# Performance work log

Hardware: AMD Instinct MI355X
Metric: run time of the kernel (lower is better)

Reference implementation:

```python
import jax, jax.numpy as jnp
import numpy as np

B, N, D_IN, D_ATTN, D_OUT = 8, 2048, 2048, 64, 2048

def setup_inputs() -> dict:
    key = jax.random.key(0)
    ks = jax.random.split(key, 5)
    x = jax.random.normal(ks[0], (B, N, D_IN), dtype=jnp.float32)
    s_qkv = 1.0 / np.sqrt(D_IN)   # torch nn.Linear default init bound
    W_qkv = jax.random.uniform(ks[1], (D_IN, 3 * D_ATTN), jnp.float32, -s_qkv, s_qkv)
    b_qkv = jax.random.uniform(ks[2], (3 * D_ATTN,), jnp.float32, -s_qkv, s_qkv)
    s_p = 1.0 / np.sqrt(D_ATTN)
    W_proj = jax.random.uniform(ks[3], (D_ATTN, D_OUT), jnp.float32, -s_p, s_p)
    b_proj = jax.random.uniform(ks[4], (D_OUT,), jnp.float32, -s_p, s_p)
    return {"x": x, "W_qkv": W_qkv, "b_qkv": b_qkv, "W_proj": W_proj, "b_proj": b_proj}

def reference(x, W_qkv, b_qkv, W_proj, b_proj):
    # qkv projection: [B,N,3*D_ATTN]
    qkv = x @ W_qkv + b_qkv
    q, k, v = jnp.split(qkv, 3, axis=-1)  # each [B,N,D_ATTN]
    scale = jax.lax.rsqrt(jnp.float32(D_ATTN))
    w = jnp.einsum('bnd,bmd->bnm', q, k) * scale  # [B,N,N]
    a = jax.nn.softmax(w, axis=-1)
    ctx = jnp.einsum('bnm,bmd->bnd', a, v)        # [B,N,D_ATTN]
    return ctx @ W_proj + b_proj                   # [B,N,D_OUT]
```

## Files before the change

### kernel.cpp

```cpp
#include <hip/hip_runtime.h>

typedef __bf16 bf16x8 __attribute__((ext_vector_type(8)));
typedef unsigned short u16x8 __attribute__((ext_vector_type(8)));
typedef unsigned short u16x4 __attribute__((ext_vector_type(4)));
typedef float  f32x4  __attribute__((ext_vector_type(4)));

#define QSCALE 0.1803368801111204f

__device__ __forceinline__ unsigned short f2bf(float f) {
  unsigned int u = __float_as_uint(f);
  u = u + 0x7fffu + ((u >> 16) & 1u);
  return (unsigned short)(u >> 16);
}

#define GLD16(src, dst)                                                        \
  __builtin_amdgcn_global_load_lds(                                            \
      (const __attribute__((address_space(1))) void*)(src),                    \
      (__attribute__((address_space(3))) void*)(dst), 16, 0, 0)


__global__ __launch_bounds__(256) void k_tr_wq(const float* __restrict__ W,
                                               unsigned short* __restrict__ WT) {
  __shared__ float tile[64][193];
  const int t = threadIdx.x;
  const int k0 = blockIdx.x * 64;
#pragma unroll
  for (int i = 0; i < 12; ++i) {
    int u = i * 256 + t;
    int row = u / 48, c4 = u % 48;
    float4 v = *(const float4*)(W + (size_t)(k0 + row) * 192 + c4 * 4);
    tile[row][c4 * 4 + 0] = v.x; tile[row][c4 * 4 + 1] = v.y;
    tile[row][c4 * 4 + 2] = v.z; tile[row][c4 * 4 + 3] = v.w;
  }
  __syncthreads();
#pragma unroll
  for (int i = 0; i < 6; ++i) {
    int u = i * 256 + t;
    int c = u >> 3, k8 = (u & 7) * 8;
    u16x8 h;
#pragma unroll
    for (int j = 0; j < 8; ++j) h[j] = f2bf(tile[k8 + j][c]);
    *(u16x8*)(WT + (size_t)c * 2048 + k0 + k8) = h;
  }
}

__global__ __launch_bounds__(256) void k_tr_wp(const float* __restrict__ W,
                                               unsigned short* __restrict__ WT) {
  __shared__ float tile[64][65];
  const int t = threadIdx.x;
  const int n0 = blockIdx.x * 64;
#pragma unroll
  for (int i = 0; i < 4; ++i) {
    int u = i * 256 + t;
    int d = u >> 4, c4 = u & 15;
    float4 v = *(const float4*)(W + (size_t)d * 2048 + n0 + c4 * 4);
    tile[d][c4 * 4 + 0] = v.x; tile[d][c4 * 4 + 1] = v.y;
    tile[d][c4 * 4 + 2] = v.z; tile[d][c4 * 4 + 3] = v.w;
  }
  __syncthreads();
#pragma unroll
  for (int i = 0; i < 2; ++i) {
    int u = i * 256 + t;
    int n = u >> 3, d8 = (u & 7) * 8;
    u16x8 h;
#pragma unroll
    for (int j = 0; j < 8; ++j) h[j] = f2bf(tile[d8 + j][n0 ? n : n]);
    h[0] = f2bf(tile[d8 + 0][n]); h[1] = f2bf(tile[d8 + 1][n]);
    h[2] = f2bf(tile[d8 + 2][n]); h[3] = f2bf(tile[d8 + 3][n]);
    h[4] = f2bf(tile[d8 + 4][n]); h[5] = f2bf(tile[d8 + 5][n]);
    h[6] = f2bf(tile[d8 + 6][n]); h[7] = f2bf(tile[d8 + 7][n]);
    *(u16x8*)(WT + (size_t)(n0 + n) * 64 + d8) = h;
  }
}

__global__ __launch_bounds__(512) void k_qkv(const float* __restrict__ x,
                                             const unsigned short* __restrict__ wqT,
                                             const float* __restrict__ b_qkv,
                                             unsigned short* __restrict__ qb,
                                             unsigned short* __restrict__ kb,
                                             unsigned short* __restrict__ vt) {
  __shared__ __align__(16) char lds[65536];
  const int t = threadIdx.x;
  const int lane = t & 63, w = t >> 6;
  const int l15 = lane & 15, l4 = lane >> 4;
  const int wm = w >> 2, wn = w & 3;
  const int m0 = blockIdx.x * 64;

  const int arow = t >> 3;
  const int akc  = (t & 7) * 8;
  const float* xrow = x + (size_t)(m0 + arow) * 2048 + akc;
  const int aoff = arow * 128 + ((akc * 2) ^ ((arow & 7) << 4));

  f32x4 acc[2][3] = {};
  float4 a0, a1;

  auto issueA = [&](int kt) {
    a0 = *(const float4*)(xrow + kt * 64);
    a1 = *(const float4*)(xrow + kt * 64 + 4);
  };
  auto writeA = [&](int d) {
    u16x8 h;
    h[0] = f2bf(a0.x); h[1] = f2bf(a0.y); h[2] = f2bf(a0.z); h[3] = f2bf(a0.w);
    h[4] = f2bf(a1.x); h[5] = f2bf(a1.y); h[6] = f2bf(a1.z); h[7] = f2bf(a1.w);
    *(u16x8*)(lds + d * 8192 + aoff) = h;
  };
  auto stageB = [&](int kt, int d) {
    char* bbase = lds + 16384 + d * 24576;
#pragma unroll
    for (int p = 0; p < 3; ++p) {
      int L = p * 8192 + (w << 10) + (lane << 4);
      int row = L >> 7;
      int cb = (L & 127) ^ ((row & 7) << 4);
      GLD16((const char*)wqT + (size_t)row * 4096 + kt * 128 + cb,
            bbase + p * 8192 + (w << 10));
    }
  };
  auto compute = [&](int d) {
    const char* aB = lds + d * 8192;
    const char* bB = lds + 16384 + d * 24576;
#pragma unroll
    for (int kk = 0; kk < 2; ++kk) {
      int cb = kk * 64 + l4 * 16;
      bf16x8 af[2], bfr[3];
#pragma unroll
      for (int m = 0; m < 2; ++m) {
        int r = wm * 32 + m * 16 + l15;
        af[m] = *(const bf16x8*)(aB + r * 128 + (cb ^ ((r & 7) << 4)));
      }
#pragma unroll
      for (int n = 0; n < 3; ++n) {
        int r = wn * 48 + n * 16 + l15;
        bfr[n] = *(const bf16x8*)(bB + r * 128 + (cb ^ ((r & 7) << 4)));
      }
#pragma unroll
      for (int m = 0; m < 2; ++m)
#pragma unroll
        for (int n = 0; n < 3; ++n)
          acc[m][n] = __builtin_amdgcn_mfma_f32_16x16x32_bf16(af[m], bfr[n], acc[m][n], 0, 0, 0);
    }
  };

  issueA(0); stageB(0, 0); writeA(0);
  __syncthreads();
  int d = 0;
  for (int kt = 0; kt < 32; ++kt) {
    if (kt < 31) { issueA(kt + 1); stageB(kt + 1, d ^ 1); }
    compute(d);
    if (kt < 31) writeA(d ^ 1);
    __syncthreads();
    d ^= 1;
  }

#pragma unroll
  for (int m = 0; m < 2; ++m)
#pragma unroll
    for (int n = 0; n < 3; ++n) {
      int c = wn * 48 + n * 16 + l15;
      int j = c >> 6, cc = c & 63;
      float bias = b_qkv[c];
      int grow0 = m0 + wm * 32 + m * 16 + l4 * 4;
      if (j == 0) {
#pragma unroll
        for (int r = 0; r < 4; ++r)
          qb[(size_t)(grow0 + r) * 64 + cc] = f2bf((acc[m][n][r] + bias) * QSCALE);
      } else if (j == 1) {
#pragma unroll
        for (int r = 0; r < 4; ++r)
          kb[(size_t)(grow0 + r) * 64 + cc] = f2bf(acc[m][n][r] + bias);
      } else {
        int bbv = grow0 >> 11, nn0 = grow0 & 2047;
        u16x4 h;
        h[0] = f2bf(acc[m][n][0] + bias); h[1] = f2bf(acc[m][n][1] + bias);
        h[2] = f2bf(acc[m][n][2] + bias); h[3] = f2bf(acc[m][n][3] + bias);
        *(u16x4*)(vt + ((size_t)bbv * 64 + cc) * 2048 + nn0) = h;
      }
    }
}

__global__ __launch_bounds__(256) void k_attn(const unsigned short* __restrict__ qb,
                                              const unsigned short* __restrict__ kb,
                                              const unsigned short* __restrict__ vt,
                                              float* __restrict__ ctxp,
                                              float* __restrict__ mlp) {
  __shared__ __align__(16) char lds[32768];
  const int t = threadIdx.x;
  const int lane = t & 63, w = t >> 6;
  const int l15 = lane & 15, l4 = lane >> 4;
  const int bb = blockIdx.y;
  const int half = blockIdx.z;
  const int q0 = blockIdx.x * 64 + w * 16;
  const int kt0 = half * 16;
  const unsigned short* qrow = qb + ((size_t)bb * 2048 + q0 + l15) * 64;
  bf16x8 aq[2];
  aq[0] = *(const bf16x8*)(qrow + l4 * 8);
  aq[1] = *(const bf16x8*)(qrow + 32 + l4 * 8);
  f32x4 ctx[4] = {};
  float m = -1e30f, lsum = 0.f;
  const char* kBase = (const char*)kb + (size_t)bb * 2048 * 128;
  const char* vBase = (const char*)vt + (size_t)bb * 64 * 4096;
  const int srcA = ((l4 & 1) << 5) | l15;
  const int srcB = srcA + 16;
  const bool hi = (l4 >> 1) & 1;

  auto stage = [&](int kt, int d) {
#pragma unroll
    for (int p = 0; p < 2; ++p) {
      int L = p * 4096 + (w << 10) + (lane << 4);
      int row = L >> 7;
      int cb = (L & 127) ^ ((row & 7) << 4);
      GLD16(kBase + (size_t)(kt * 64 + row) * 128 + cb,
            lds + d * 8192 + p * 4096 + (w << 10));
      GLD16(vBase + (size_t)row * 4096 + kt * 128 + cb,
            lds + 16384 + d * 8192 + p * 4096 + (w << 10));
    }
  };

  stage(kt0, 0);
  __syncthreads();
  int d = 0;
  for (int kt = 0; kt < 16; ++kt) {
    if (kt < 15) stage(kt0 + kt + 1, d ^ 1);
    const char* sK = lds + d * 8192;
    const char* sV = lds + 16384 + d * 8192;
    f32x4 s[4] = {};
    __builtin_amdgcn_s_setprio(1);
#pragma unroll
    for (int kk = 0; kk < 2; ++kk) {
      int cb = kk * 64 + l4 * 16;
#pragma unroll
      for (int mf = 0; mf < 4; ++mf) {
        int r = mf * 16 + l15;
        bf16x8 kf = *(const bf16x8*)(sK + r * 128 + (cb ^ ((r & 7) << 4)));
        s[mf] = __builtin_amdgcn_mfma_f32_16x16x32_bf16(kf, aq[kk], s[mf], 0, 0, 0);
      }
    }
    __builtin_amdgcn_s_setprio(0);
    float pm = fmaxf(fmaxf(fmaxf(s[0][0], s[0][1]), fmaxf(s[0][2], s[0][3])),
                     fmaxf(fmaxf(s[1][0], s[1][1]), fmaxf(s[1][2], s[1][3])));
    pm = fmaxf(pm, fmaxf(fmaxf(fmaxf(s[2][0], s[2][1]), fmaxf(s[2][2], s[2][3])),
                         fmaxf(fmaxf(s[3][0], s[3][1]), fmaxf(s[3][2], s[3][3]))));
    pm = fmaxf(pm, __shfl_xor(pm, 16));
    pm = fmaxf(pm, __shfl_xor(pm, 32));
    if (!__all(pm <= m + 11.5f)) {
      float mn = fmaxf(m, pm);
      float al = __builtin_exp2f(m - mn);
      m = mn; lsum *= al;
#pragma unroll
      for (int df = 0; df < 4; ++df)
#pragma unroll
        for (int r = 0; r < 4; ++r) ctx[df][r] *= al;
    }
    float lp = 0.f;
#pragma unroll
    for (int mf = 0; mf < 4; ++mf)
#pragma unroll
      for (int r = 0; r < 4; ++r) {
        float p = __builtin_exp2f(s[mf][r] - m);
        s[mf][r] = p;
        lp += p;
      }
    lsum += lp;
    unsigned int pk[4][2];
#pragma unroll
    for (int mf = 0; mf < 4; ++mf) {
      asm("v_cvt_pk_bf16_f32 %0, %1, %2" : "=v"(pk[mf][0]) : "v"(s[mf][0]), "v"(s[mf][1]));
      asm("v_cvt_pk_bf16_f32 %0, %1, %2" : "=v"(pk[mf][1]) : "v"(s[mf][2]), "v"(s[mf][3]));
    }
#pragma unroll
    for (int kk = 0; kk < 2; ++kk) {
      unsigned int q00 = __shfl((int)pk[2 * kk][0], srcA);
      unsigned int q10 = __shfl((int)pk[2 * kk + 1][0], srcA);
      unsigned int q01 = __shfl((int)pk[2 * kk][1], srcA);
      unsigned int q11 = __shfl((int)pk[2 * kk + 1][1], srcA);
      unsigned int r00 = __shfl((int)pk[2 * kk][0], srcB);
      unsigned int r10 = __shfl((int)pk[2 * kk + 1][0], srcB);
      unsigned int r01 = __shfl((int)pk[2 * kk][1], srcB);
      unsigned int r11 = __shfl((int)pk[2 * kk + 1][1], srcB);
      uint4 uu;
      uu.x = hi ? q10 : q00;
      uu.y = hi ? q11 : q01;
      uu.z = hi ? r10 : r00;
      uu.w = hi ? r11 : r01;
      bf16x8 pfrag = *(bf16x8*)&uu;
      int cb = kk * 64 + l4 * 16;
      __builtin_amdgcn_s_setprio(1);
#pragma unroll
      for (int df = 0; df < 4; ++df) {
        int rv = df * 16 + l15;
        bf16x8 vf = *(const bf16x8*)(sV + rv * 128 + (cb ^ ((rv & 7) << 4)));
        ctx[df] = __builtin_amdgcn_mfma_f32_16x16x32_bf16(vf, pfrag, ctx[df], 0, 0, 0);
      }
      __builtin_amdgcn_s_setprio(0);
    }
    __syncthreads();
    d ^= 1;
  }
  lsum += __shfl_xor(lsum, 16);
  lsum += __shfl_xor(lsum, 32);
  size_t g = (size_t)bb * 2048 + q0 + l15;
#pragma unroll
  for (int df = 0; df < 4; ++df) {
    f32x4 c = ctx[df];
    *(float4*)(ctxp + ((size_t)half * 16384 + g) * 64 + df * 16 + l4 * 4) =
        *(float4*)&c;
  }
  if (l4 == 0) {
    float2 ml = make_float2(m, lsum);
    *(float2*)(mlp + ((size_t)half * 16384 + g) * 2) = ml;
  }
}

__global__ __launch_bounds__(256) void k_proj(const float* __restrict__ ctxp,
                                              const float* __restrict__ mlp,
                                              const unsigned short* __restrict__ wpT,
                                              const float* __restrict__ b_proj,
                                              float* __restrict__ out) {
  __shared__ __align__(16) char lds[40960];
  const int t = threadIdx.x;
  const int lane = t & 63, w = t >> 6;
  const int l15 = lane & 15, l4 = lane >> 4;
  const int m0 = blockIdx.x * 64;
  const int n0 = blockIdx.y * 256;

  {
    int r_ = t >> 2;
    int dq = (t & 3) << 4;
    size_t g = (size_t)m0 + r_;
    float m0v = mlp[g * 2], l0v = mlp[g * 2 + 1];
    float m1v = mlp[((size_t)16384 + g) * 2], l1v = mlp[((size_t)16384 + g) * 2 + 1];
    float M = fmaxf(m0v, m1v);
    float a0 = __builtin_exp2f(m0v - M), a1 = __builtin_exp2f(m1v - M);
    float inv = 1.0f / (l0v * a0 + l1v * a1);
    a0 *= inv; a1 *= inv;
    const float4* h0 = (const float4*)(ctxp + g * 64 + dq);
    const float4* h1 = (const float4*)(ctxp + ((size_t)16384 + g) * 64 + dq);
    int sw = (r_ & 7) << 4;
#pragma unroll
    for (int q = 0; q < 2; ++q) {
      float4 v0a = h0[q * 2], v0b = h0[q * 2 + 1];
      float4 v1a = h1[q * 2], v1b = h1[q * 2 + 1];
      u16x8 o;
      o[0] = f2bf(v0a.x * a0 + v1a.x * a1); o[1] = f2bf(v0a.y * a0 + v1a.y * a1);
      o[2] = f2bf(v0a.z * a0 + v1a.z * a1); o[3] = f2bf(v0a.w * a0 + v1a.w * a1);
      o[4] = f2bf(v0b.x * a0 + v1b.x * a1); o[5] = f2bf(v0b.y * a0 + v1b.y * a1);
      o[6] = f2bf(v0b.z * a0 + v1b.z * a1); o[7] = f2bf(v0b.w * a0 + v1b.w * a1);
      *(u16x8*)(lds + r_ * 128 + ((dq * 2 + q * 16) ^ sw)) = o;
    }
  }
#pragma unroll
  for (int p = 0; p < 8; ++p) {
    int L = p * 4096 + t * 16;
    int row = L >> 7;
    int cb = (L & 127) ^ ((row & 7) << 4);
    GLD16((const char*)wpT + (size_t)(n0 + row) * 128 + cb,
          lds + 8192 + p * 4096 + (w << 10));
  }
  __syncthreads();

  f32x4 acc[4][4] = {};
#pragma unroll
  for (int kk = 0; kk < 2; ++kk) {
    int cb = kk * 64 + l4 * 16;
    bf16x8 af[4], bfr[4];
#pragma unroll
    for (int m = 0; m < 4; ++m) {
      int r = m * 16 + l15;
      af[m] = *(const bf16x8*)(lds + r * 128 + (cb ^ ((r & 7) << 4)));
    }
#pragma unroll
    for (int n = 0; n < 4; ++n) {
      int r = w * 64 + n * 16 + l15;
      bfr[n] = *(const bf16x8*)(lds + 8192 + r * 128 + (cb ^ ((r & 7) << 4)));
    }
#pragma unroll
    for (int m = 0; m < 4; ++m)
#pragma unroll
      for (int n = 0; n < 4; ++n)
        acc[m][n] = __builtin_amdgcn_mfma_f32_16x16x32_bf16(bfr[n], af[m], acc[m][n], 0, 0, 0);
  }
#pragma unroll
  for (int m = 0; m < 4; ++m)
#pragma unroll
    for (int n = 0; n < 4; ++n) {
      int grow = m0 + m * 16 + l15;
      int gcol = n0 + w * 64 + n * 16 + l4 * 4;
      float4 bias = *(const float4*)(b_proj + gcol);
      float4 o;
      o.x = acc[m][n][0] + bias.x; o.y = acc[m][n][1] + bias.y;
      o.z = acc[m][n][2] + bias.z; o.w = acc[m][n][3] + bias.w;
      *(float4*)(out + (size_t)grow * 2048 + gcol) = o;
    }
}

extern "C" void kernel_launch(void* const* d_in, const int* in_sizes, int n_in,
                              void* d_out, int out_size, void* d_ws, size_t ws_size,
                              hipStream_t stream) {
  const float* x      = (const float*)d_in[0];
  const float* W_qkv  = (const float*)d_in[1];
  const float* b_qkv  = (const float*)d_in[2];
  const float* W_proj = (const float*)d_in[3];
  const float* b_proj = (const float*)d_in[4];
  float* out = (float*)d_out;

  unsigned short* ws   = (unsigned short*)d_ws;
  unsigned short* wqT  = ws;
  unsigned short* wpT  = wqT + (size_t)192 * 2048;
  unsigned short* qb   = wpT + (size_t)2048 * 64;
  unsigned short* kb   = qb  + (size_t)16384 * 64;
  unsigned short* vt   = kb  + (size_t)16384 * 64;
  float* ctxp = (float*)(vt + (size_t)16384 * 64);
  float* mlp  = ctxp + (size_t)2 * 16384 * 64;

  k_tr_wq<<<32, 256, 0, stream>>>(W_qkv, wqT);
  k_tr_wp<<<32, 256, 0, stream>>>(W_proj, wpT);
  k_qkv<<<256, 512, 0, stream>>>(x, wqT, b_qkv, qb, kb, vt);
  k_attn<<<dim3(32, 8, 2), 256, 0, stream>>>(qb, kb, vt, ctxp, mlp);
  k_proj<<<dim3(256, 8), 256, 0, stream>>>(ctxp, mlp, wpT, b_proj, out);
}
```

Baseline: 111.9 us.

## Merge weight transposes and deepen QKV pipeline with explicit vmcnt waits

Combines the two weight-transpose kernels into one launch to remove a kernel launch. In the QKV GEMM, it double-buffers the x register prefetch two tiles ahead and swaps __syncthreads for explicit s_waitcnt vmcnt counts plus raw barriers, with setprio raised around the MFMA compute. The attention kernel likewise waits only on the older stage's loads before its barrier. Hand-counted vmcnt values are fragile: if the compiler reorders or adds memory ops, they can become wrong and cause races.

```diff
diff --git a/kernel.cpp b/kernel.cpp
--- a/kernel.cpp
+++ b/kernel.cpp
@@ -19,57 +19,54 @@
       (__attribute__((address_space(3))) void*)(dst), 16, 0, 0)
 
 
-__global__ __launch_bounds__(256) void k_tr_wq(const float* __restrict__ W,
-                                               unsigned short* __restrict__ WT) {
+__global__ __launch_bounds__(256) void k_trw(const float* __restrict__ Wq,
+                                             const float* __restrict__ Wp,
+                                             unsigned short* __restrict__ wqT,
+                                             unsigned short* __restrict__ wpT) {
   __shared__ float tile[64][193];
   const int t = threadIdx.x;
-  const int k0 = blockIdx.x * 64;
-#pragma unroll
-  for (int i = 0; i < 12; ++i) {
-    int u = i * 256 + t;
-    int row = u / 48, c4 = u % 48;
-    float4 v = *(const float4*)(W + (size_t)(k0 + row) * 192 + c4 * 4);
-    tile[row][c4 * 4 + 0] = v.x; tile[row][c4 * 4 + 1] = v.y;
-    tile[row][c4 * 4 + 2] = v.z; tile[row][c4 * 4 + 3] = v.w;
-  }
-  __syncthreads();
-#pragma unroll
-  for (int i = 0; i < 6; ++i) {
-    int u = i * 256 + t;
-    int c = u >> 3, k8 = (u & 7) * 8;
-    u16x8 h;
-#pragma unroll
-    for (int j = 0; j < 8; ++j) h[j] = f2bf(tile[k8 + j][c]);
-    *(u16x8*)(WT + (size_t)c * 2048 + k0 + k8) = h;
-  }
-}
-
-__global__ __launch_bounds__(256) void k_tr_wp(const float* __restrict__ W,
-                                               unsigned short* __restrict__ WT) {
-  __shared__ float tile[64][65];
-  const int t = threadIdx.x;
-  const int n0 = blockIdx.x * 64;
-#pragma unroll
-  for (int i = 0; i < 4; ++i) {
-    int u = i * 256 + t;
-    int d = u >> 4, c4 = u & 15;
-    float4 v = *(const float4*)(W + (size_t)d * 2048 + n0 + c4 * 4);
-    tile[d][c4 * 4 + 0] = v.x; tile[d][c4 * 4 + 1] = v.y;
-    tile[d][c4 * 4 + 2] = v.z; tile[d][c4 * 4 + 3] = v.w;
-  }
-  __syncthreads();
-#pragma unroll
-  for (int i = 0; i < 2; ++i) {
-    int u = i * 256 + t;
-    int n = u >> 3, d8 = (u & 7) * 8;
-    u16x8 h;
-#pragma unroll
-    for (int j = 0; j < 8; ++j) h[j] = f2bf(tile[d8 + j][n0 ? n : n]);
-    h[0] = f2bf(tile[d8 + 0][n]); h[1] = f2bf(tile[d8 + 1][n]);
-    h[2] = f2bf(tile[d8 + 2][n]); h[3] = f2bf(tile[d8 + 3][n]);
-    h[4] = f2bf(tile[d8 + 4][n]); h[5] = f2bf(tile[d8 + 5][n]);
-    h[6] = f2bf(tile[d8 + 6][n]); h[7] = f2bf(tile[d8 + 7][n]);
-    *(u16x8*)(WT + (size_t)(n0 + n) * 64 + d8) = h;
+  if (blockIdx.x < 32) {
+    const int k0 = blockIdx.x * 64;
+#pragma unroll
+    for (int i = 0; i < 12; ++i) {
+      int u = i * 256 + t;
+      int row = u / 48, c4 = u % 48;
+      float4 v = *(const float4*)(Wq + (size_t)(k0 + row) * 192 + c4 * 4);
+      tile[row][c4 * 4 + 0] = v.x; tile[row][c4 * 4 + 1] = v.y;
+      tile[row][c4 * 4 + 2] = v.z; tile[row][c4 * 4 + 3] = v.w;
+    }
+    __syncthreads();
+#pragma unroll
+    for (int i = 0; i < 6; ++i) {
+      int u = i * 256 + t;
+      int c = u >> 3, k8 = (u & 7) * 8;
+      u16x8 h;
+#pragma unroll
+      for (int j = 0; j < 8; ++j) h[j] = f2bf(tile[k8 + j][c]);
+      *(u16x8*)(wqT + (size_t)c * 2048 + k0 + k8) = h;
+    }
+  } else {
+    const int n0 = (blockIdx.x - 32) * 64;
+#pragma unroll
+    for (int i = 0; i < 4; ++i) {
+      int u = i * 256 + t;
+      int dd = u >> 4, c4 = u & 15;
+      float4 v = *(const float4*)(Wp + (size_t)dd * 2048 + n0 + c4 * 4);
+      tile[dd][c4 * 4 + 0] = v.x; tile[dd][c4 * 4 + 1] = v.y;
+      tile[dd][c4 * 4 + 2] = v.z; tile[dd][c4 * 4 + 3] = v.w;
+    }
+    __syncthreads();
+#pragma unroll
+    for (int i = 0; i < 2; ++i) {
+      int u = i * 256 + t;
+      int n = u >> 3, d8 = (u & 7) * 8;
+      u16x8 h;
+      h[0] = f2bf(tile[d8 + 0][n]); h[1] = f2bf(tile[d8 + 1][n]);
+      h[2] = f2bf(tile[d8 + 2][n]); h[3] = f2bf(tile[d8 + 3][n]);
+      h[4] = f2bf(tile[d8 + 4][n]); h[5] = f2bf(tile[d8 + 5][n]);
+      h[6] = f2bf(tile[d8 + 6][n]); h[7] = f2bf(tile[d8 + 7][n]);
+      *(u16x8*)(wpT + (size_t)(n0 + n) * 64 + d8) = h;
+    }
   }
 }
 
@@ -92,17 +89,27 @@
   const int aoff = arow * 128 + ((akc * 2) ^ ((arow & 7) << 4));
 
   f32x4 acc[2][3] = {};
-  float4 a0, a1;
-
-  auto issueA = [&](int kt) {
-    a0 = *(const float4*)(xrow + kt * 64);
-    a1 = *(const float4*)(xrow + kt * 64 + 4);
-  };
-  auto writeA = [&](int d) {
+  float4 xa0_0, xa1_0, xa0_1, xa1_1;
+
+  auto issueA_0 = [&](int kt) {
+    xa0_0 = *(const float4*)(xrow + kt * 64);
+    xa1_0 = *(const float4*)(xrow + kt * 64 + 4);
+  };
+  auto issueA_1 = [&](int kt) {
+    xa0_1 = *(const float4*)(xrow + kt * 64);
+    xa1_1 = *(const float4*)(xrow + kt * 64 + 4);
+  };
+  auto writeA_0 = [&]() {
     u16x8 h;
-    h[0] = f2bf(a0.x); h[1] = f2bf(a0.y); h[2] = f2bf(a0.z); h[3] = f2bf(a0.w);
-    h[4] = f2bf(a1.x); h[5] = f2bf(a1.y); h[6] = f2bf(a1.z); h[7] = f2bf(a1.w);
-    *(u16x8*)(lds + d * 8192 + aoff) = h;
+    h[0] = f2bf(xa0_0.x); h[1] = f2bf(xa0_0.y); h[2] = f2bf(xa0_0.z); h[3] = f2bf(xa0_0.w);
+    h[4] = f2bf(xa1_0.x); h[5] = f2bf(xa1_0.y); h[6] = f2bf(xa1_0.z); h[7] = f2bf(xa1_0.w);
+    *(u16x8*)(lds + 0 * 8192 + aoff) = h;
+  };
+  auto writeA_1 = [&]() {
+    u16x8 h;
+    h[0] = f2bf(xa0_1.x); h[1] = f2bf(xa0_1.y); h[2] = f2bf(xa0_1.z); h[3] = f2bf(xa0_1.w);
+    h[4] = f2bf(xa1_1.x); h[5] = f2bf(xa1_1.y); h[6] = f2bf(xa1_1.z); h[7] = f2bf(xa1_1.w);
+    *(u16x8*)(lds + 1 * 8192 + aoff) = h;
   };
   auto stageB = [&](int kt, int d) {
     char* bbase = lds + 16384 + d * 24576;
@@ -118,6 +125,7 @@
   auto compute = [&](int d) {
     const char* aB = lds + d * 8192;
     const char* bB = lds + 16384 + d * 24576;
+    __builtin_amdgcn_s_setprio(1);
 #pragma unroll
     for (int kk = 0; kk < 2; ++kk) {
       int cb = kk * 64 + l4 * 16;
@@ -138,18 +146,28 @@
         for (int n = 0; n < 3; ++n)
           acc[m][n] = __builtin_amdgcn_mfma_f32_16x16x32_bf16(af[m], bfr[n], acc[m][n], 0, 0, 0);
     }
-  };
-
-  issueA(0); stageB(0, 0); writeA(0);
-  __syncthreads();
-  int d = 0;
-  for (int kt = 0; kt < 32; ++kt) {
-    if (kt < 31) { issueA(kt + 1); stageB(kt + 1, d ^ 1); }
-    compute(d);
-    if (kt < 31) writeA(d ^ 1);
-    __syncthreads();
-    d ^= 1;
-  }
+    __builtin_amdgcn_s_setprio(0);
+  };
+
+#define QKV_STEP(n, P, DOI, DOS, W)                                    \
+  {                                                                    \
+    writeA_##P();                                                      \
+    if (DOI) issueA_##P((n) + 2);                                      \
+    if (DOS) stageB((n) + 1, (P) ^ 1);                                 \
+    asm volatile("s_waitcnt vmcnt(" W ") lgkmcnt(0)" ::: "memory");    \
+    __builtin_amdgcn_s_barrier();                                      \
+    compute(P);                                                        \
+    __builtin_amdgcn_s_barrier();                                      \
+  }
+
+  issueA_0(0); issueA_1(1); stageB(0, 0);
+  for (int kt = 0; kt < 30; kt += 2) {
+    QKV_STEP(kt,     0, true, true, "5");
+    QKV_STEP(kt + 1, 1, true, true, "5");
+  }
+  QKV_STEP(30, 0, false, true,  "5");
+  QKV_STEP(31, 1, false, false, "0");
+#undef QKV_STEP
 
 #pragma unroll
   for (int m = 0; m < 2; ++m)
@@ -216,10 +234,15 @@
   };
 
   stage(kt0, 0);
-  __syncthreads();
   int d = 0;
   for (int kt = 0; kt < 16; ++kt) {
-    if (kt < 15) stage(kt0 + kt + 1, d ^ 1);
+    if (kt < 15) {
+      stage(kt0 + kt + 1, d ^ 1);
+      asm volatile("s_waitcnt vmcnt(4)" ::: "memory");
+    } else {
+      asm volatile("s_waitcnt vmcnt(0)" ::: "memory");
+    }
+    __builtin_amdgcn_s_barrier();
     const char* sK = lds + d * 8192;
     const char* sV = lds + 16384 + d * 8192;
     f32x4 s[4] = {};
@@ -292,7 +315,7 @@
       }
       __builtin_amdgcn_s_setprio(0);
     }
-    __syncthreads();
+    __builtin_amdgcn_s_barrier();
     d ^= 1;
   }
   lsum += __shfl_xor(lsum, 16);
@@ -411,8 +434,7 @@
   float* ctxp = (float*)(vt + (size_t)16384 * 64);
   float* mlp  = ctxp + (size_t)2 * 16384 * 64;
 
-  k_tr_wq<<<32, 256, 0, stream>>>(W_qkv, wqT);
-  k_tr_wp<<<32, 256, 0, stream>>>(W_proj, wpT);
+  k_trw<<<64, 256, 0, stream>>>(W_qkv, W_proj, wqT, wpT);
   k_qkv<<<256, 512, 0, stream>>>(x, wqT, b_qkv, qb, kb, vt);
   k_attn<<<dim3(32, 8, 2), 256, 0, stream>>>(qb, kb, vt, ctxp, mlp);
   k_proj<<<dim3(256, 8), 256, 0, stream>>>(ctxp, mlp, wpT, b_proj, out);
```

New measurement: 104.5 us. 6.6% less time.
